# Optimization experiments

Hardware: AMD Instinct MI355X
Metric: run time of the kernel (lower is better)

Reference implementation:

```python
import jax, jax.numpy as jnp
import numpy as np

B, H, KVH, D = 32, 32, 8, 128
BS = 128                      # KV-cache block size
BLOCKS_PER_SEQ = 14
NB = B * BLOCKS_PER_SEQ       # 448 active blocks
NUM_CACHE_BLOCKS = 512
CTX = 13 * BS + 64            # 1728 tokens per sequence (incl. new decode token)
SCALE = 0.08838834764831845   # 1/sqrt(head_size)
NEG = -1e9


def _slopes(n):
    return (2.0 ** (-8.0 / n * np.arange(1, n + 1))).astype(np.float32)


def setup_inputs() -> dict:
    key = jax.random.key(0)
    ks = jax.random.split(key, 5)
    query = jax.random.normal(ks[0], (B, 1, H * D), dtype=jnp.float32)
    key_t = jax.random.normal(ks[1], (B, 1, KVH * D), dtype=jnp.float32)
    value = jax.random.normal(ks[2], (B, 1, KVH * D), dtype=jnp.float32)
    key_cache = jax.random.normal(ks[3], (NUM_CACHE_BLOCKS, BS, KVH, D), dtype=jnp.float32)
    value_cache = jax.random.normal(ks[4], (NUM_CACHE_BLOCKS, BS, KVH, D), dtype=jnp.float32)

    block_list = np.arange(NB, dtype=np.int32)                      # cache block id per active block (seq-major)
    block_groups = np.repeat(np.arange(B, dtype=np.int32), BLOCKS_PER_SEQ)
    block_mapping = np.zeros((NB, B), dtype=np.float32)             # one-hot block->batch map
    block_mapping[np.arange(NB), block_groups] = 1.0

    valid = CTX - 13 * BS                                           # 64 valid slots in last block
    block_bias = np.zeros((NB, BS), dtype=np.float32)
    last = np.arange(B) * BLOCKS_PER_SEQ + (BLOCKS_PER_SEQ - 1)
    block_bias[last, valid:] = NEG

    # alibi distances per kv slot: (kv_pos - (CTX-1)); zero on masked slots
    pos_in_seq = (np.tile(np.arange(BLOCKS_PER_SEQ), B)[:, None] * BS
                  + np.arange(BS)[None, :]).astype(np.float32)
    alibi_blocks = np.where(block_bias < 0, 0.0, pos_in_seq - float(CTX - 1)).astype(np.float32)

    block_indices = last.astype(np.int32)                           # write new token into last block
    block_offsets = np.full((B,), valid - 1, dtype=np.int32)

    return {"query": query, "key": key_t, "value": value,
            "key_cache": key_cache, "value_cache": value_cache,
            "block_list": jnp.asarray(block_list), "block_groups": jnp.asarray(block_groups),
            "block_mapping": jnp.asarray(block_mapping), "block_bias": jnp.asarray(block_bias),
            "block_indices": jnp.asarray(block_indices), "block_offsets": jnp.asarray(block_offsets),
            "alibi_blocks": jnp.asarray(alibi_blocks), "alibi_slopes": jnp.asarray(_slopes(H))}


def reference(query, key, value, key_cache, value_cache, block_list, block_groups,
              block_mapping, block_bias, block_indices, block_offsets,
              alibi_blocks, alibi_slopes):
    G = H // KVH                                                    # queries per kv head
    q = query.reshape(B, H, D)
    k_new = key.reshape(B, KVH, D)
    v_new = value.reshape(B, KVH, D)
    # KV-cache insertion of the new decode token (VLLMKVCache insert)
    key_cache = key_cache.at[block_indices, block_offsets].set(k_new)
    value_cache = value_cache.at[block_indices, block_offsets].set(v_new)
    # batch2block: replicate each sequence's query to its blocks via one-hot matmul
    q_blk = jnp.einsum('nb,bhd->nhd', block_mapping, SCALE * q).reshape(NB, KVH, G, D)
    k = key_cache[block_list]                                       # [NB, BS, KVH, D] paged fetch
    v = value_cache[block_list]
    attn = jnp.einsum('nkgd,nskd->nkgs', q_blk, k)                  # [NB, KVH, G, BS]
    # decode alibi bias: slopes * per-slot distance, grouped for GQA
    pos_bias = (alibi_blocks[:, None, :] * alibi_slopes[None, :, None]).reshape(NB, KVH, G, BS)
    attn = attn + pos_bias + block_bias[:, None, None, :]
    # grouped (per-sequence) numerically-stable softmax across blocks
    block_max = jnp.max(attn, axis=-1)                              # [NB, KVH, G]
    group_max = jax.ops.segment_max(block_max, block_groups, num_segments=B)
    m = jax.lax.stop_gradient(group_max[block_groups])
    p = jnp.exp(attn - m[..., None])
    block_sum = jnp.sum(p, axis=-1)                                 # [NB, KVH, G]
    o_blk = jnp.einsum('nkgs,nskd->nkgd', p, v)                     # [NB, KVH, G, D]
    # block2batch: accumulate block partials back per sequence
    o = jnp.einsum('nb,nkgd->bkgd', block_mapping, o_blk)
    s = jnp.einsum('nb,nkg->bkg', block_mapping, block_sum)
    out = o / s[..., None]
    return out.reshape(B, 1, H * D)
```

## Files before the change

### kernel.cpp

```cpp
#include <hip/hip_runtime.h>
#include <stdint.h>

#define B_    32
#define H_    32
#define KVH_  8
#define D_    128
#define BS_   128
#define BPS_  14
#define NB_   448
#define G_    4
#define CHUNK_ 32
#define SCALE_ 0.08838834764831845f

__device__ __forceinline__ void g2lds16(const float* gp, float* lp) {
  __builtin_amdgcn_global_load_lds(
      (__attribute__((address_space(1))) void*)gp,
      (__attribute__((address_space(3))) void*)lp,
      16, 0, 0);
}

__global__ __launch_bounds__(256) void kv_insert_kernel(
    const float* __restrict__ knew, const float* __restrict__ vnew,
    float* __restrict__ kc, float* __restrict__ vc,
    const int* __restrict__ bidx, const int* __restrict__ boff) {
  int b = blockIdx.x, t = threadIdx.x;
  size_t dst = ((size_t)bidx[b] * BS_ + (size_t)boff[b]) * (KVH_ * D_);
  const float4* sk = (const float4*)(knew + (size_t)b * KVH_ * D_);
  const float4* sv = (const float4*)(vnew + (size_t)b * KVH_ * D_);
  ((float4*)(kc + dst))[t] = sk[t];
  ((float4*)(vc + dst))[t] = sv[t];
}

__global__ __launch_bounds__(256) void attn_part_kernel(
    const float* __restrict__ query,
    const float* __restrict__ kc, const float* __restrict__ vc,
    const int* __restrict__ block_list, const int* __restrict__ block_groups,
    const float* __restrict__ block_bias, const float* __restrict__ alibi_blocks,
    const float* __restrict__ alibi_slopes,
    float* __restrict__ p_o, float* __restrict__ p_m, float* __restrict__ p_l) {
  __shared__ float smem[2 * CHUNK_ * D_];
  __shared__ float q_s[G_ * D_];
  __shared__ float attn_s[G_ * BS_];
  __shared__ float bias_s[BS_];
  __shared__ float alibi_s[BS_];

  const int bid = blockIdx.x;
  const int n = bid >> 3, kvh = bid & 7;
  const int t = threadIdx.x;
  const int lane = t & 63, wv = t >> 6;
  const int s_loc = lane & 31, dh = lane >> 5;

  const int cb = block_list[n];
  const int b  = block_groups[n];
  const int nch = (n % BPS_ == BPS_ - 1) ? 2 : 4;

  const float* kbase = kc + ((size_t)cb * BS_ * KVH_ + kvh) * D_;
  const float* vbase = vc + ((size_t)cb * BS_ * KVH_ + kvh) * D_;

  {
    int r = wv * 8;
    #pragma unroll
    for (int i = 0; i < 4; ++i) {
      const float* g = kbase + (size_t)(r + 2 * i + dh) * (KVH_ * D_) + s_loc * 4;
      g2lds16(g, smem + (r + 2 * i) * D_);
    }
  }
  if (t < 128) {
    float4 qv = *(const float4*)(query + (size_t)b * (H_ * D_) +
                                 (size_t)kvh * (G_ * D_) + (size_t)t * 4);
    qv.x *= SCALE_; qv.y *= SCALE_; qv.z *= SCALE_; qv.w *= SCALE_;
    ((float4*)q_s)[t] = qv;
  } else {
    int i = t - 128;
    bias_s[i]  = block_bias[(size_t)n * BS_ + i];
    alibi_s[i] = alibi_blocks[(size_t)n * BS_ + i];
  }
  const float slope = alibi_slopes[kvh * G_ + wv];
  __syncthreads();

  const int rot = s_loc & 15;

  for (int c = 0; c < nch; ++c) {
    {
      int p1 = c + 1;
      const float* base = (p1 < nch) ? kbase : vbase;
      int ch = (p1 < nch) ? p1 : 0;
      float* dst = smem + (p1 & 1) * (CHUNK_ * D_);
      int r = wv * 8;
      #pragma unroll
      for (int i = 0; i < 4; ++i) {
        const float* g = base + (size_t)(ch * CHUNK_ + r + 2 * i + dh) * (KVH_ * D_) + s_loc * 4;
        g2lds16(g, dst + (r + 2 * i) * D_);
      }
    }
    float acc = 0.f;
    const float4* kb = (const float4*)(smem + (c & 1) * (CHUNK_ * D_) + s_loc * D_ + dh * 64);
    const float4* qb = (const float4*)(q_s + wv * D_ + dh * 64);
    #pragma unroll
    for (int j = 0; j < 16; ++j) {
      int jj = (j + rot) & 15;
      float4 kvv = kb[jj];
      float4 qv = qb[jj];
      acc += kvv.x * qv.x + kvv.y * qv.y + kvv.z * qv.z + kvv.w * qv.w;
    }
    acc += __shfl_xor(acc, 32);
    if (lane < 32) {
      int s = c * CHUNK_ + s_loc;
      attn_s[wv * BS_ + s] = acc + slope * alibi_s[s] + bias_s[s];
    }
    __syncthreads();
  }

  {
    float a0 = attn_s[wv * BS_ + lane];
    float a1 = (nch == 4) ? attn_s[wv * BS_ + 64 + lane] : -1e30f;
    float mx = fmaxf(a0, a1);
    #pragma unroll
    for (int off = 32; off > 0; off >>= 1) mx = fmaxf(mx, __shfl_xor(mx, off));
    float p0 = __expf(a0 - mx);
    float p1 = __expf(a1 - mx);
    attn_s[wv * BS_ + lane] = p0;
    if (nch == 4) attn_s[wv * BS_ + 64 + lane] = p1;
    float sm = p0 + p1;
    #pragma unroll
    for (int off = 32; off > 0; off >>= 1) sm += __shfl_xor(sm, off);
    if (lane == 0) {
      p_m[(size_t)bid * G_ + wv] = mx;
      p_l[(size_t)bid * G_ + wv] = sm;
    }
  }
  __syncthreads();

  const int col4 = (lane & 31) * 4;
  const int rh = lane >> 5;
  float4 acc4[G_];
  #pragma unroll
  for (int g = 0; g < G_; ++g) acc4[g] = make_float4(0.f, 0.f, 0.f, 0.f);

  for (int c = 0; c < nch; ++c) {
    int p = nch + c;
    if (c + 1 < nch) {
      float* dst = smem + ((p + 1) & 1) * (CHUNK_ * D_);
      int r = wv * 8;
      #pragma unroll
      for (int i = 0; i < 4; ++i) {
        const float* g = vbase + (size_t)((c + 1) * CHUNK_ + r + 2 * i + dh) * (KVH_ * D_) + s_loc * 4;
        g2lds16(g, dst + (r + 2 * i) * D_);
      }
    }
    const float* vb = smem + (p & 1) * (CHUNK_ * D_);
    #pragma unroll
    for (int i = 0; i < 4; ++i) {
      int rloc = wv * 8 + i * 2 + rh;
      float4 v4 = *(const float4*)(vb + rloc * D_ + col4);
      int s = c * CHUNK_ + rloc;
      #pragma unroll
      for (int g = 0; g < G_; ++g) {
        float pg = attn_s[g * BS_ + s];
        acc4[g].x += pg * v4.x;
        acc4[g].y += pg * v4.y;
        acc4[g].z += pg * v4.z;
        acc4[g].w += pg * v4.w;
      }
    }
    __syncthreads();
  }

  float* red = smem;
  {
    int part = wv * 2 + rh;
    #pragma unroll
    for (int g = 0; g < G_; ++g)
      *(float4*)&red[part * (G_ * D_) + g * D_ + col4] = acc4[g];
  }
  __syncthreads();
  {
    int g = t >> 6;
    int d = (t & 63) * 2;
    float2 sum = make_float2(0.f, 0.f);
    #pragma unroll
    for (int w = 0; w < 8; ++w) {
      float2 r = *(const float2*)&red[w * (G_ * D_) + g * D_ + d];
      sum.x += r.x; sum.y += r.y;
    }
    *(float2*)(p_o + ((size_t)bid * G_ + g) * D_ + d) = sum;
  }
}

__global__ __launch_bounds__(256) void attn_reduce_kernel(
    const float* __restrict__ p_o, const float* __restrict__ p_m,
    const float* __restrict__ p_l, float* __restrict__ out) {
  int bk = blockIdx.x;
  int b = bk >> 3, kvh = bk & 7;
  int t = threadIdx.x;
  int g = t >> 6, lane = t & 63;
  int d = lane * 2;

  float M = -1e30f;
  #pragma unroll
  for (int i = 0; i < BPS_; ++i) {
    size_t pid = ((size_t)(b * BPS_ + i) * KVH_ + kvh) * G_ + g;
    M = fmaxf(M, p_m[pid]);
  }
  float denom = 0.f;
  float2 acc = make_float2(0.f, 0.f);
  #pragma unroll
  for (int i = 0; i < BPS_; ++i) {
    size_t pid = ((size_t)(b * BPS_ + i) * KVH_ + kvh) * G_ + g;
    float w = __expf(p_m[pid] - M);
    denom += w * p_l[pid];
    float2 o = *(const float2*)(p_o + pid * D_ + d);
    acc.x += w * o.x;
    acc.y += w * o.y;
  }
  float inv = 1.f / denom;
  float2 r = make_float2(acc.x * inv, acc.y * inv);
  *(float2*)(out + (size_t)b * (H_ * D_) + (size_t)(kvh * G_ + g) * D_ + d) = r;
}

extern "C" void kernel_launch(void* const* d_in, const int* in_sizes, int n_in,
                              void* d_out, int out_size, void* d_ws, size_t ws_size,
                              hipStream_t stream) {
  const float* query = (const float*)d_in[0];
  const float* key   = (const float*)d_in[1];
  const float* value = (const float*)d_in[2];
  float* kc          = (float*)d_in[3];
  float* vc          = (float*)d_in[4];
  const int* block_list    = (const int*)d_in[5];
  const int* block_groups  = (const int*)d_in[6];
  const float* block_bias  = (const float*)d_in[8];
  const int* bidx          = (const int*)d_in[9];
  const int* boff          = (const int*)d_in[10];
  const float* alibi_blocks = (const float*)d_in[11];
  const float* alibi_slopes = (const float*)d_in[12];
  float* out = (float*)d_out;

  const size_t n_po = (size_t)NB_ * KVH_ * G_ * D_;
  const size_t n_pm = (size_t)NB_ * KVH_ * G_;
  const size_t need = (n_po + 2 * n_pm) * sizeof(float);
  float* scratch = (ws_size >= need) ? (float*)d_ws
                                     : kc + (size_t)NB_ * BS_ * KVH_ * D_;
  float* p_o = scratch;
  float* p_m = scratch + n_po;
  float* p_l = p_m + n_pm;

  kv_insert_kernel<<<B_, 256, 0, stream>>>(key, value, kc, vc, bidx, boff);
  attn_part_kernel<<<NB_ * KVH_, 256, 0, stream>>>(
      query, kc, vc, block_list, block_groups, block_bias,
      alibi_blocks, alibi_slopes, p_o, p_m, p_l);
  attn_reduce_kernel<<<B_ * KVH_, 256, 0, stream>>>(p_o, p_m, p_l, out);
}
```

Before: 516.2 us.

## Load V directly from global into registers instead of LDS double-buffering

The PV phase now has each half-wave load 16 V rows straight from global memory into registers, in two batches of 8 float4 loads. This replaces the chunked LDS double-buffer and removes the per-chunk __syncthreads. The K loop no longer prefetches the first V chunk, and launch bounds request 4 blocks per CU. The goal is more loads in flight and less sync overhead, at the cost of more registers and losing the V prefetch overlapped with the QK phase.

```diff
diff --git a/kernel.cpp b/kernel.cpp
--- a/kernel.cpp
+++ b/kernel.cpp
@@ -31,7 +31,7 @@
   ((float4*)(vc + dst))[t] = sv[t];
 }
 
-__global__ __launch_bounds__(256) void attn_part_kernel(
+__global__ __launch_bounds__(256, 4) void attn_part_kernel(
     const float* __restrict__ query,
     const float* __restrict__ kc, const float* __restrict__ vc,
     const int* __restrict__ block_list, const int* __restrict__ block_groups,
@@ -81,15 +81,12 @@
   const int rot = s_loc & 15;
 
   for (int c = 0; c < nch; ++c) {
-    {
-      int p1 = c + 1;
-      const float* base = (p1 < nch) ? kbase : vbase;
-      int ch = (p1 < nch) ? p1 : 0;
-      float* dst = smem + (p1 & 1) * (CHUNK_ * D_);
+    if (c + 1 < nch) {
+      float* dst = smem + ((c + 1) & 1) * (CHUNK_ * D_);
       int r = wv * 8;
       #pragma unroll
       for (int i = 0; i < 4; ++i) {
-        const float* g = base + (size_t)(ch * CHUNK_ + r + 2 * i + dh) * (KVH_ * D_) + s_loc * 4;
+        const float* g = kbase + (size_t)((c + 1) * CHUNK_ + r + 2 * i + dh) * (KVH_ * D_) + s_loc * 4;
         g2lds16(g, dst + (r + 2 * i) * D_);
       }
     }
@@ -132,46 +129,40 @@
   __syncthreads();
 
   const int col4 = (lane & 31) * 4;
-  const int rh = lane >> 5;
+  const int group = wv * 2 + (lane >> 5);
   float4 acc4[G_];
   #pragma unroll
   for (int g = 0; g < G_; ++g) acc4[g] = make_float4(0.f, 0.f, 0.f, 0.f);
 
-  for (int c = 0; c < nch; ++c) {
-    int p = nch + c;
-    if (c + 1 < nch) {
-      float* dst = smem + ((p + 1) & 1) * (CHUNK_ * D_);
-      int r = wv * 8;
+  if (group < nch * 2) {
+    #pragma unroll
+    for (int half = 0; half < 2; ++half) {
+      float4 v4[8];
       #pragma unroll
-      for (int i = 0; i < 4; ++i) {
-        const float* g = vbase + (size_t)((c + 1) * CHUNK_ + r + 2 * i + dh) * (KVH_ * D_) + s_loc * 4;
-        g2lds16(g, dst + (r + 2 * i) * D_);
+      for (int i = 0; i < 8; ++i) {
+        int s = group * 16 + half * 8 + i;
+        v4[i] = *(const float4*)(vbase + (size_t)s * (KVH_ * D_) + col4);
       }
-    }
-    const float* vb = smem + (p & 1) * (CHUNK_ * D_);
-    #pragma unroll
-    for (int i = 0; i < 4; ++i) {
-      int rloc = wv * 8 + i * 2 + rh;
-      float4 v4 = *(const float4*)(vb + rloc * D_ + col4);
-      int s = c * CHUNK_ + rloc;
       #pragma unroll
-      for (int g = 0; g < G_; ++g) {
-        float pg = attn_s[g * BS_ + s];
-        acc4[g].x += pg * v4.x;
-        acc4[g].y += pg * v4.y;
-        acc4[g].z += pg * v4.z;
-        acc4[g].w += pg * v4.w;
+      for (int i = 0; i < 8; ++i) {
+        int s = group * 16 + half * 8 + i;
+        #pragma unroll
+        for (int g = 0; g < G_; ++g) {
+          float pg = attn_s[g * BS_ + s];
+          acc4[g].x += pg * v4[i].x;
+          acc4[g].y += pg * v4[i].y;
+          acc4[g].z += pg * v4[i].z;
+          acc4[g].w += pg * v4[i].w;
+        }
       }
     }
-    __syncthreads();
   }
 
   float* red = smem;
   {
-    int part = wv * 2 + rh;
     #pragma unroll
     for (int g = 0; g < G_; ++g)
-      *(float4*)&red[part * (G_ * D_) + g * D_ + col4] = acc4[g];
+      *(float4*)&red[group * (G_ * D_) + g * D_ + col4] = acc4[g];
   }
   __syncthreads();
   {
```

Result: no change. 519.4 us (+0.6%).
